# Optimization experiments

Measured on AMD Instinct MI355X. Metric: run time of the kernel, lower is better.

## Reference

```python
import jax, jax.numpy as jnp
import numpy as np

# Model dims (match init_kwargs / Mamba2 defaults)
D_MODEL = 1024
D_STATE = 128
D_CONV = 4
EXPAND = 2
HEADDIM = 64
NGROUPS = 1
D_INNER = EXPAND * D_MODEL            # 2048
NHEADS = D_INNER // HEADDIM           # 32
D_IN_PROJ = 2 * D_INNER + 2 * NGROUPS * D_STATE + NHEADS  # 4384 (d_mlp == 0)
CONV_DIM = D_INNER + 2 * NGROUPS * D_STATE                 # 2304
BATCH = 2
SEQLEN = 512
EPS = 1e-5


def _silu(x):
    return x * jax.nn.sigmoid(x)


def setup_inputs() -> dict:
    key = jax.random.key(0)
    ks = jax.random.split(key, 8)
    u = jax.random.normal(ks[0], (BATCH, SEQLEN, D_MODEL), jnp.float32)
    W_in = jax.random.normal(ks[1], (D_IN_PROJ, D_MODEL), jnp.float32) * (D_MODEL ** -0.5)
    conv_w = jax.random.normal(ks[2], (CONV_DIM, 1, D_CONV), jnp.float32) * (D_CONV ** -0.5)
    conv_b = jnp.zeros((CONV_DIM,), jnp.float32)
    # dt_bias init as in the torch module (inverse-softplus of dt in [dt_min, dt_max])
    dt = jnp.exp(jax.random.uniform(ks[3], (NHEADS,), jnp.float32)
                 * (np.log(0.1) - np.log(0.001)) + np.log(0.001))
    dt = jnp.clip(dt, 1e-4, None)
    dt_bias = dt + jnp.log(-jnp.expm1(-dt))
    A_log = jnp.log(jax.random.uniform(ks[4], (NHEADS,), jnp.float32, minval=1.0, maxval=16.0))
    D_param = jnp.ones((NHEADS,), jnp.float32)
    norm_w = jnp.ones((D_INNER,), jnp.float32)
    W_out = jax.random.normal(ks[5], (D_MODEL, D_INNER), jnp.float32) * (D_INNER ** -0.5)
    return dict(u=u, W_in=W_in, conv_w=conv_w, conv_b=conv_b, dt_bias=dt_bias,
                A_log=A_log, D_param=D_param, norm_w=norm_w, W_out=W_out)


def reference(u, W_in, conv_w, conv_b, dt_bias, A_log, D_param, norm_w, W_out):
    B, L, _ = u.shape
    # in_proj (no bias): [B,L,d_in_proj]
    zxbcdt = jnp.einsum('bld,ed->ble', u, W_in)
    z = zxbcdt[..., :D_INNER]
    xBC = zxbcdt[..., D_INNER:D_INNER + CONV_DIM]
    dt = zxbcdt[..., D_INNER + CONV_DIM:]          # [B,L,H]

    # causal depthwise conv1d (pad left d_conv-1 == conv padding + slice in torch)
    xc = jnp.transpose(xBC, (0, 2, 1))             # [B,C,L]
    xc = jax.lax.conv_general_dilated(
        xc, conv_w, window_strides=(1,), padding=[(D_CONV - 1, 0)],
        dimension_numbers=('NCH', 'OIH', 'NCH'), feature_group_count=CONV_DIM)
    xc = xc + conv_b[None, :, None]
    xBC = _silu(jnp.transpose(xc, (0, 2, 1)))      # [B,L,C]

    x = xBC[..., :D_INNER].reshape(B, L, NHEADS, HEADDIM)
    Bv = xBC[..., D_INNER:D_INNER + NGROUPS * D_STATE].reshape(B, L, NGROUPS, D_STATE)
    Cv = xBC[..., D_INNER + NGROUPS * D_STATE:].reshape(B, L, NGROUPS, D_STATE)

    A = -jnp.exp(A_log)                            # [H]
    dt = jax.nn.softplus(dt + dt_bias)             # [B,L,H]

    def step(state, inp):
        dt_t, x_t, B_t, C_t = inp                  # [B,H],[B,H,P],[B,G,N],[B,G,N]
        dA = jnp.exp(dt_t * A)                     # [B,H]
        dBx = jnp.einsum('bh,bgn,bhp->bhpn', dt_t, B_t, x_t)
        state = state * dA[:, :, None, None] + dBx
        y = jnp.einsum('bhpn,bgn->bhp', state, C_t) + D_param[:, None] * x_t
        return state, y

    state0 = jnp.zeros((B, NHEADS, HEADDIM, D_STATE), u.dtype)
    xs = (jnp.moveaxis(dt, 1, 0), jnp.moveaxis(x, 1, 0),
          jnp.moveaxis(Bv, 1, 0), jnp.moveaxis(Cv, 1, 0))
    _, ys = jax.lax.scan(step, state0, xs)         # ys: [L,B,H,P]
    y = jnp.moveaxis(ys, 0, 1).reshape(B, L, D_INNER)

    # RMSNormGated, norm_before_gate=False: gate first, then rmsnorm
    yg = y * _silu(z)
    yn = yg * jax.lax.rsqrt(jnp.mean(yg * yg, axis=-1, keepdims=True) + EPS) * norm_w

    return jnp.einsum('bld,ed->ble', yn, W_out)    # out_proj, no bias
```

## Files before the change

kernel.cpp:

```cpp
#include <hip/hip_runtime.h>
#include <hip/hip_bf16.h>

#define D_MODEL   1024
#define D_STATE   128
#define D_INNER   2048
#define NHEADS    32
#define HEADDIM   64
#define D_IN_PROJ 4384
#define NPROJ_PAD 4480
#define CONV_DIM  2304
#define BATCH     2
#define SEQLEN    512
#define M_TOKENS  (BATCH*SEQLEN)
#define EPS       1e-5f
#define LC        64
#define NCH       (SEQLEN/LC)

typedef __bf16 bf16x8 __attribute__((ext_vector_type(8)));
typedef float  f32x4  __attribute__((ext_vector_type(4)));

__device__ __forceinline__ ushort f2bf(float f) {
  union { float f; unsigned int i; } v; v.f = f;
  unsigned int x = v.i;
  return (ushort)((x + 0x7fffu + ((x >> 16) & 1u)) >> 16);
}
__device__ __forceinline__ float bf2f(ushort u) {
  union { unsigned int i; float f; } v; v.i = ((unsigned int)u) << 16; return v.f;
}

__device__ __forceinline__ void gload_lds16u(const ushort* g, ushort* l) {
  __builtin_amdgcn_global_load_lds(
      (const __attribute__((address_space(1))) void*)g,
      (__attribute__((address_space(3))) void*)l, 16, 0, 0);
}

__device__ __forceinline__ void cvt8(const float* __restrict__ s,
                                     ushort* __restrict__ d, int i) {
  const float4 a = *(const float4*)(s + i);
  const float4 b = *(const float4*)(s + i + 4);
  uint4 v;
  v.x = (unsigned)f2bf(a.x) | ((unsigned)f2bf(a.y) << 16);
  v.y = (unsigned)f2bf(a.z) | ((unsigned)f2bf(a.w) << 16);
  v.z = (unsigned)f2bf(b.x) | ((unsigned)f2bf(b.y) << 16);
  v.w = (unsigned)f2bf(b.z) | ((unsigned)f2bf(b.w) << 16);
  *(uint4*)(d + i) = v;
}
__global__ __launch_bounds__(256) void cvt3(const float* __restrict__ s0, ushort* __restrict__ d0, int n0,
                                            const float* __restrict__ s1, ushort* __restrict__ d1, int n1,
                                            const float* __restrict__ s2, ushort* __restrict__ d2, int n2,
                                            const float* __restrict__ nw) {
  const int i = (blockIdx.x * 256 + threadIdx.x) * 8;
  if (i < n0)           cvt8(s0, d0, i);
  else if (i < n0 + n1) cvt8(s1, d1, i - n0);
  else if (i < n0 + n1 + n2) {
    const int j = i - n0 - n1;
    const int k = j & (D_INNER - 1);
    const float4 a = *(const float4*)(s2 + j);
    const float4 b = *(const float4*)(s2 + j + 4);
    const float4 wa = *(const float4*)(nw + k);
    const float4 wb = *(const float4*)(nw + k + 4);
    uint4 v;
    v.x = (unsigned)f2bf(a.x * wa.x) | ((unsigned)f2bf(a.y * wa.y) << 16);
    v.y = (unsigned)f2bf(a.z * wa.z) | ((unsigned)f2bf(a.w * wa.w) << 16);
    v.z = (unsigned)f2bf(b.x * wb.x) | ((unsigned)f2bf(b.y * wb.y) << 16);
    v.w = (unsigned)f2bf(b.z * wb.z) | ((unsigned)f2bf(b.w * wb.w) << 16);
    *(uint4*)(d2 + j) = v;
  }
}

template <int BM, int BN, int MASK_N>
__global__ __launch_bounds__(256) void gemm_tile(const ushort* __restrict__ A,
                                                 const ushort* __restrict__ Bt,
                                                 float* __restrict__ C,
                                                 int Nreal, int K, int ldc) {
  constexpr int WM = BM / 2, WN = BN / 2, FM = WM / 16, FN = WN / 16;
  constexpr int LA = BM * 4 / 256, LB = BN * 4 / 256;
  __shared__ ushort As[BM * 32];
  __shared__ ushort Bs[BN * 32];
  const int tid = threadIdx.x, lane = tid & 63, wave = tid >> 6;
  const int r16 = lane & 15, q = lane >> 4;
  const int wm = wave & 1, wn = wave >> 1;
  const int m0 = blockIdx.y * BM, n0 = blockIdx.x * BN;

  f32x4 acc[FM][FN] = {};

  for (int k0 = 0; k0 < K; k0 += 32) {
    __syncthreads();
    #pragma unroll
    for (int it = 0; it < LA; ++it) {
      const int idx = it * 256 + tid;
      gload_lds16u(A + (size_t)(m0 + (idx >> 2)) * K + k0 + (idx & 3) * 8,
                   As + (it * 256 + wave * 64) * 8);
    }
    #pragma unroll
    for (int it = 0; it < LB; ++it) {
      const int idx = it * 256 + tid;
      gload_lds16u(Bt + (size_t)(n0 + (idx >> 2)) * K + k0 + (idx & 3) * 8,
                   Bs + (it * 256 + wave * 64) * 8);
    }
    __syncthreads();

    bf16x8 af[FM], bfr[FN];
    #pragma unroll
    for (int i = 0; i < FM; ++i)
      af[i] = *(const bf16x8*)(const void*)(As + (wm * WM + i * 16 + r16) * 32 + q * 8);
    #pragma unroll
    for (int j = 0; j < FN; ++j)
      bfr[j] = *(const bf16x8*)(const void*)(Bs + (wn * WN + j * 16 + r16) * 32 + q * 8);
    #pragma unroll
    for (int i = 0; i < FM; ++i)
      #pragma unroll
      for (int j = 0; j < FN; ++j)
        acc[i][j] = __builtin_amdgcn_mfma_f32_16x16x32_bf16(af[i], bfr[j], acc[i][j], 0, 0, 0);
  }

  #pragma unroll
  for (int i = 0; i < FM; ++i) {
    const int row = m0 + wm * WM + i * 16 + q * 4;
    #pragma unroll
    for (int j = 0; j < FN; ++j) {
      const int col = n0 + wn * WN + j * 16 + r16;
      if (!MASK_N || col < Nreal) {
        #pragma unroll
        for (int r = 0; r < 4; ++r)
          C[(size_t)(row + r) * ldc + col] = acc[i][j][r];
      }
    }
  }
}

__global__ __launch_bounds__(256) void gemm_sk(const ushort* __restrict__ A,
                                               const ushort* __restrict__ Bt,
                                               float* __restrict__ C,
                                               const float* __restrict__ sumsq,
                                               int Khalf, int ldab, int ldc) {
  __shared__ ushort As[64 * 32];
  __shared__ ushort Bs[64 * 32];
  const int tid = threadIdx.x, lane = tid & 63, wave = tid >> 6;
  const int r16 = lane & 15, q = lane >> 4;
  const int wm = wave & 1, wn = wave >> 1;
  const int m0 = blockIdx.y * 64, n0 = blockIdx.x * 64;
  const int kb = blockIdx.z * Khalf;

  f32x4 acc[2][2] = {};
  for (int k0 = 0; k0 < Khalf; k0 += 32) {
    __syncthreads();
    gload_lds16u(A + (size_t)(m0 + (tid >> 2)) * ldab + kb + k0 + (tid & 3) * 8,
                 As + (tid & ~63) * 8);
    gload_lds16u(Bt + (size_t)(n0 + (tid >> 2)) * ldab + kb + k0 + (tid & 3) * 8,
                 Bs + (tid & ~63) * 8);
    __syncthreads();

    bf16x8 af[2], bfr[2];
    #pragma unroll
    for (int i = 0; i < 2; ++i)
      af[i] = *(const bf16x8*)(const void*)(As + (wm * 32 + i * 16 + r16) * 32 + q * 8);
    #pragma unroll
    for (int j = 0; j < 2; ++j)
      bfr[j] = *(const bf16x8*)(const void*)(Bs + (wn * 32 + j * 16 + r16) * 32 + q * 8);
    #pragma unroll
    for (int i = 0; i < 2; ++i)
      #pragma unroll
      for (int j = 0; j < 2; ++j)
        acc[i][j] = __builtin_amdgcn_mfma_f32_16x16x32_bf16(af[i], bfr[j], acc[i][j], 0, 0, 0);
  }

  #pragma unroll
  for (int i = 0; i < 2; ++i) {
    const int row = m0 + wm * 32 + i * 16 + q * 4;
    float rms[4];
    #pragma unroll
    for (int r = 0; r < 4; ++r)
      rms[r] = rsqrtf(sumsq[row + r] * (1.f / D_INNER) + EPS);
    #pragma unroll
    for (int j = 0; j < 2; ++j) {
      const int col = n0 + wn * 32 + j * 16 + r16;
      #pragma unroll
      for (int r = 0; r < 4; ++r)
        unsafeAtomicAdd(&C[(size_t)(row + r) * ldc + col], acc[i][j][r] * rms[r]);
    }
  }
}

__global__ __launch_bounds__(256) void conv_dt(const float* __restrict__ zx,
                                               const float* __restrict__ cw,
                                               const float* __restrict__ cb,
                                               float* __restrict__ xbc,
                                               ushort* __restrict__ BCbf,
                                               const float* __restrict__ dt_bias,
                                               const float* __restrict__ A_log,
                                               float* __restrict__ dts,
                                               float* __restrict__ csum) {
  const int blk = blockIdx.x;
  if (blk < 1152) {
    const int g  = blk / 9;
    const int c  = (blk % 9) * 256 + threadIdx.x;
    const int b  = g >> 6;
    const int t0 = (g & 63) * 8;
    const float4 w4 = *(const float4*)(cw + c * 4);
    const float bias = cb[c];
    const float* col = zx + (size_t)(b * SEQLEN) * D_IN_PROJ + D_INNER + c;
    float win[11];
    #pragma unroll
    for (int k = 0; k < 11; ++k) {
      const int t = t0 - 3 + k;
      win[k] = (t >= 0) ? col[(size_t)t * D_IN_PROJ] : 0.f;
    }
    #pragma unroll
    for (int i = 0; i < 8; ++i) {
      float a = bias;
      a = fmaf(win[i],     w4.x, a);
      a = fmaf(win[i + 1], w4.y, a);
      a = fmaf(win[i + 2], w4.z, a);
      a = fmaf(win[i + 3], w4.w, a);
      const float s = a / (1.f + __expf(-a));
      const size_t bt = (size_t)(b * SEQLEN + t0 + i);
      xbc[bt * CONV_DIM + c] = s;
      if (c >= D_INNER) BCbf[bt * 256 + (c - D_INNER)] = f2bf(s);
    }
  } else {
    const int bh = blk - 1152;
    const int b = bh >> 5, h = bh & 31;
    const int wave = threadIdx.x >> 6, lane = threadIdx.x & 63;
    const float dtb = dt_bias[h];
    const float An  = -__expf(A_log[h]);
    for (int cc = wave; cc < NCH; cc += 4) {
      const int t = cc * LC + lane;
      const float raw = zx[(size_t)(b * SEQLEN + t) * D_IN_PROJ + (D_INNER + CONV_DIM) + h] + dtb;
      const float sp = (raw > 20.f) ? raw : log1pf(__expf(raw));
      float x = sp * An;
      #pragma unroll
      for (int off = 1; off < 64; off <<= 1) {
        const float v = __shfl_up(x, off);
        if (lane >= off) x += v;
      }
      dts[(size_t)bh * SEQLEN + t]  = sp;
      csum[(size_t)bh * SEQLEN + t] = x;
    }
  }
}

__global__ __launch_bounds__(256) void chunk_intra(const float* __restrict__ xbc,
                                                   const ushort* __restrict__ BCbf,
                                                   const float* __restrict__ dts,
                                                   const float* __restrict__ csum,
                                                   ushort* __restrict__ Yi,
                                                   ushort* __restrict__ dS) {
  const int blk = blockIdx.x;
  const int c = blk & 7, h = (blk >> 3) & 31, b = blk >> 8;
  const int bh = b * 32 + h;
  const int tid = threadIdx.x, lane = tid & 63, wave = tid >> 6;
  const int r16 = lane & 15, q = lane >> 4;

  __shared__ ushort Ml[64 * 72];
  __shared__ ushort Xt[64 * 72];
  __shared__ ushort Bw[128 * 72];
  __shared__ float dtl[LC], csl[LC];

  if (tid < LC) {
    dtl[tid] = dts[(size_t)bh * SEQLEN + c * LC + tid];
    csl[tid] = csum[(size_t)bh * SEQLEN + c * LC + tid];
  }
  __syncthreads();
  const float cs63 = csl[LC - 1];

  const ushort* Cp = BCbf + (size_t)(b * SEQLEN + c * LC + wave * 16 + r16) * 256 + 128 + q * 8;
  const ushort* Bp = BCbf + (size_t)(b * SEQLEN + c * LC + r16) * 256 + q * 8;
  f32x4 g[4] = {};
  #pragma unroll
  for (int kk = 0; kk < 4; ++kk) {
    const bf16x8 a = *(const bf16x8*)(const void*)(Cp + kk * 32);
    #pragma unroll
    for (int j = 0; j < 4; ++j) {
      const bf16x8 bb = *(const bf16x8*)(const void*)(Bp + (size_t)j * 16 * 256 + kk * 32);
      g[j] = __builtin_amdgcn_mfma_f32_16x16x32_bf16(a, bb, g[j], 0, 0, 0);
    }
  }
  float cst[4];
  #pragma unroll
  for (int r = 0; r < 4; ++r) cst[r] = csl[wave * 16 + q * 4 + r];
  #pragma unroll
  for (int j = 0; j < 4; ++j) {
    const int s = j * 16 + r16;
    const float ds_ = dtl[s], css = csl[s];
    #pragma unroll
    for (int r = 0; r < 4; ++r) {
      const int t = wave * 16 + q * 4 + r;
      const float v = (s <= t) ? g[j][r] * ds_ * __expf(cst[r] - css) : 0.f;
      Ml[t * 72 + s] = f2bf(v);
    }
  }

  const float* xb = xbc + (size_t)(b * SEQLEN + c * LC) * CONV_DIM + h * HEADDIM;
  #pragma unroll
  for (int i = 0; i < 16; ++i) {
    const int idx = i * 256 + tid;
    const int s = idx >> 6, p = idx & 63;
    Xt[p * 72 + s] = f2bf(xb[(size_t)s * CONV_DIM + p]);
  }
  const float* Bb = xbc + (size_t)(b * SEQLEN + c * LC) * CONV_DIM + D_INNER;
  #pragma unroll
  for (int i = 0; i < 32; ++i) {
    const int idx = i * 256 + tid;
    const int s = idx >> 7, n = idx & 127;
    const float w = dtl[s] * __expf(cs63 - csl[s]);
    Bw[n * 72 + s] = f2bf(Bb[(size_t)s * CONV_DIM + n] * w);
  }
  __syncthreads();

  f32x4 accY[4] = {};
  f32x4 accS[2][4] = {};
  #pragma unroll
  for (int kk = 0; kk < 2; ++kk) {
    const bf16x8 am = *(const bf16x8*)(const void*)(Ml + (wave * 16 + r16) * 72 + kk * 32 + q * 8);
    const bf16x8 a0 = *(const bf16x8*)(const void*)(Bw + (wave * 32 + r16) * 72 + kk * 32 + q * 8);
    const bf16x8 a1 = *(const bf16x8*)(const void*)(Bw + (wave * 32 + 16 + r16) * 72 + kk * 32 + q * 8);
    #pragma unroll
    for (int j = 0; j < 4; ++j) {
      const bf16x8 bx = *(const bf16x8*)(const void*)(Xt + (j * 16 + r16) * 72 + kk * 32 + q * 8);
      accY[j]    = __builtin_amdgcn_mfma_f32_16x16x32_bf16(am, bx, accY[j], 0, 0, 0);
      accS[0][j] = __builtin_amdgcn_mfma_f32_16x16x32_bf16(a0, bx, accS[0][j], 0, 0, 0);
      accS[1][j] = __builtin_amdgcn_mfma_f32_16x16x32_bf16(a1, bx, accS[1][j], 0, 0, 0);
    }
  }

  ushort* Yp = Yi + (size_t)blk * 4096;
  #pragma unroll
  for (int j = 0; j < 4; ++j)
    #pragma unroll
    for (int r = 0; r < 4; ++r)
      Yp[(wave * 16 + q * 4 + r) * 64 + j * 16 + r16] = f2bf(accY[j][r]);

  ushort* Sp = dS + (size_t)blk * 8192;
  #pragma unroll
  for (int u = 0; u < 2; ++u)
    #pragma unroll
    for (int j = 0; j < 4; ++j)
      #pragma unroll
      for (int r = 0; r < 4; ++r)
        Sp[(wave * 32 + u * 16 + q * 4 + r) * 64 + j * 16 + r16] = f2bf(accS[u][j][r]);
}

__global__ __launch_bounds__(256) void chunk_state(const ushort* __restrict__ dS,
                                                   const float* __restrict__ csum,
                                                   ushort* __restrict__ St) {
  const int bh = blockIdx.x;
  const int tid = threadIdx.x;
  const int p = tid & 63, n0 = (tid >> 6) * 32;
  float S[32] = {};
  for (int c = 0; c < NCH; ++c) {
    const size_t base = ((size_t)bh * 8 + c) * 8192;
    uint4 pk[4];
    unsigned* pw = (unsigned*)pk;
    #pragma unroll
    for (int j = 0; j < 16; ++j)
      pw[j] = (unsigned)f2bf(S[2 * j]) | ((unsigned)f2bf(S[2 * j + 1]) << 16);
    uint4* dst = (uint4*)(St + base + (size_t)p * 128 + n0);
    #pragma unroll
    for (int j = 0; j < 4; ++j) dst[j] = pk[j];
    const float e = __expf(csum[(size_t)bh * SEQLEN + c * LC + (LC - 1)]);
    #pragma unroll
    for (int j = 0; j < 32; ++j) {
      const float d = bf2f(dS[base + (size_t)(n0 + j) * 64 + p]);
      S[j] = S[j] * e + d;
    }
  }
}

__global__ __launch_bounds__(256) void chunk_inter(const ushort* __restrict__ BCbf,
                                                   const ushort* __restrict__ St,
                                                   const ushort* __restrict__ Yi,
                                                   const float* __restrict__ xbc,
                                                   const float* __restrict__ zx,
                                                   const float* __restrict__ csum,
                                                   const float* __restrict__ Dp,
                                                   ushort* __restrict__ yn,
                                                   float* __restrict__ sumsq) {
  const int blk = blockIdx.x;
  const int c = blk & 7, h = (blk >> 3) & 31, b = blk >> 8;
  const int bh = b * 32 + h;
  const int tid = threadIdx.x, lane = tid & 63, wave = tid >> 6;
  const int r16 = lane & 15, q = lane >> 4;

  const ushort* Cp = BCbf + (size_t)(b * SEQLEN + c * LC + wave * 16 + r16) * 256 + 128 + q * 8;
  const ushort* Sp = St + (size_t)blk * 8192 + (size_t)r16 * 128 + q * 8;
  f32x4 acc[4] = {};
  #pragma unroll
  for (int kk = 0; kk < 4; ++kk) {
    const bf16x8 a = *(const bf16x8*)(const void*)(Cp + kk * 32);
    #pragma unroll
    for (int j = 0; j < 4; ++j) {
      const bf16x8 bb = *(const bf16x8*)(const void*)(Sp + (size_t)j * 16 * 128 + kk * 32);
      acc[j] = __builtin_amdgcn_mfma_f32_16x16x32_bf16(a, bb, acc[j], 0, 0, 0);
    }
  }

  const float Dh = Dp[h];
  const ushort* Yp = Yi + (size_t)blk * 4096;
  float sc[4], ssq[4] = {0.f, 0.f, 0.f, 0.f};
  #pragma unroll
  for (int r = 0; r < 4; ++r)
    sc[r] = __expf(csum[(size_t)bh * SEQLEN + c * LC + wave * 16 + q * 4 + r]);
  #pragma unroll
  for (int j = 0; j < 4; ++j) {
    const int col = j * 16 + r16;
    #pragma unroll
    for (int r = 0; r < 4; ++r) {
      const int t = wave * 16 + q * 4 + r;
      const size_t row = (size_t)(b * SEQLEN + c * LC + t);
      const float xv = xbc[row * CONV_DIM + h * HEADDIM + col];
      const float yv = acc[j][r] * sc[r] + bf2f(Yp[t * 64 + col]) + Dh * xv;
      const float z  = zx[row * D_IN_PROJ + h * HEADDIM + col];
      const float yg = yv * (z / (1.f + __expf(-z)));
      yn[row * D_INNER + h * HEADDIM + col] = f2bf(yg);
      ssq[r] = fmaf(yg, yg, ssq[r]);
    }
  }
  #pragma unroll
  for (int o = 1; o < 16; o <<= 1) {
    #pragma unroll
    for (int r = 0; r < 4; ++r) ssq[r] += __shfl_xor(ssq[r], o);
  }
  if (r16 == 0) {
    #pragma unroll
    for (int r = 0; r < 4; ++r) {
      const int t = wave * 16 + q * 4 + r;
      unsafeAtomicAdd(&sumsq[b * SEQLEN + c * LC + t], ssq[r]);
    }
  }
}

extern "C" void kernel_launch(void* const* d_in, const int* in_sizes, int n_in,
                              void* d_out, int out_size, void* d_ws, size_t ws_size,
                              hipStream_t stream) {
  const float* u       = (const float*)d_in[0];
  const float* W_in    = (const float*)d_in[1];
  const float* conv_w  = (const float*)d_in[2];
  const float* conv_b  = (const float*)d_in[3];
  const float* dt_bias = (const float*)d_in[4];
  const float* A_log   = (const float*)d_in[5];
  const float* D_par   = (const float*)d_in[6];
  const float* norm_w  = (const float*)d_in[7];
  const float* W_out   = (const float*)d_in[8];
  float* out = (float*)d_out;

  char* ws = (char*)d_ws;
  float*  zx      = (float*)ws;
  float*  xbc     = (float*)(ws + 17956864);
  float*  sumsq   = (float*)(ws + 27394048);
  ushort* yn      = (ushort*)(ws + 35782656);
  ushort* u_bf    = (ushort*)(ws + 39976960);
  ushort* Win_bf  = (ushort*)(ws + 42074112);
  ushort* Yi      = (ushort*)(ws + 39976960);
  ushort* Wout_bf = (ushort*)(ws + 51052544);
  ushort* BC_bf   = (ushort*)(ws + 55246848);
  float*  dts     = (float*)(ws + 55771136);
  float*  csum    = (float*)(ws + 55902208);
  ushort* dS      = (ushort*)(ws + 56295424);
  ushort* St      = (ushort*)(ws + 64684032);

  hipMemsetAsync(out, 0, (size_t)M_TOKENS * D_MODEL * sizeof(float), stream);
  hipMemsetAsync(sumsq, 0, (size_t)M_TOKENS * sizeof(float), stream);

  const int n_u = M_TOKENS * D_MODEL, n_wi = D_IN_PROJ * D_MODEL, n_wo = D_MODEL * D_INNER;
  cvt3<<<(n_u + n_wi + n_wo) / (256 * 8), 256, 0, stream>>>(
      u, u_bf, n_u, W_in, Win_bf, n_wi, W_out, Wout_bf, n_wo, norm_w);

  gemm_tile<128, 64, 1><<<dim3(NPROJ_PAD / 64, M_TOKENS / 128), 256, 0, stream>>>(
      u_bf, Win_bf, zx, D_IN_PROJ, D_MODEL, D_IN_PROJ);
  conv_dt<<<1152 + 64, 256, 0, stream>>>(zx, conv_w, conv_b, xbc, BC_bf,
                                         dt_bias, A_log, dts, csum);

  chunk_intra<<<BATCH * NHEADS * NCH, 256, 0, stream>>>(xbc, BC_bf, dts, csum, Yi, dS);
  chunk_state<<<BATCH * NHEADS, 256, 0, stream>>>(dS, csum, St);
  chunk_inter<<<BATCH * NHEADS * NCH, 256, 0, stream>>>(BC_bf, St, Yi, xbc, zx,
                                                        csum, D_par, yn, sumsq);

  gemm_sk<<<dim3(D_MODEL / 64, M_TOKENS / 64, 2), 256, 0, stream>>>(
      yn, Wout_bf, out, sumsq, D_INNER / 2, D_INNER, D_MODEL);
}
```

Before: 188.9 us.

## Fold chunk-state recurrence into chunk_inter and double K-step in GEMMs

Measured after the change: 171.5 us. -9.2%, faster.

```diff
diff --git a/kernel.cpp b/kernel.cpp
--- a/kernel.cpp
+++ b/kernel.cpp
@@ -75,8 +75,8 @@
                                                  int Nreal, int K, int ldc) {
   constexpr int WM = BM / 2, WN = BN / 2, FM = WM / 16, FN = WN / 16;
   constexpr int LA = BM * 4 / 256, LB = BN * 4 / 256;
-  __shared__ ushort As[BM * 32];
-  __shared__ ushort Bs[BN * 32];
+  __shared__ ushort As[2 * BM * 32];
+  __shared__ ushort Bs[2 * BN * 32];
   const int tid = threadIdx.x, lane = tid & 63, wave = tid >> 6;
   const int r16 = lane & 15, q = lane >> 4;
   const int wm = wave & 1, wn = wave >> 1;
@@ -84,34 +84,40 @@
 
   f32x4 acc[FM][FN] = {};
 
-  for (int k0 = 0; k0 < K; k0 += 32) {
+  for (int k0 = 0; k0 < K; k0 += 64) {
     __syncthreads();
     #pragma unroll
-    for (int it = 0; it < LA; ++it) {
-      const int idx = it * 256 + tid;
-      gload_lds16u(A + (size_t)(m0 + (idx >> 2)) * K + k0 + (idx & 3) * 8,
-                   As + (it * 256 + wave * 64) * 8);
-    }
-    #pragma unroll
-    for (int it = 0; it < LB; ++it) {
-      const int idx = it * 256 + tid;
-      gload_lds16u(Bt + (size_t)(n0 + (idx >> 2)) * K + k0 + (idx & 3) * 8,
-                   Bs + (it * 256 + wave * 64) * 8);
+    for (int pp = 0; pp < 2; ++pp) {
+      #pragma unroll
+      for (int it = 0; it < LA; ++it) {
+        const int idx = it * 256 + tid;
+        gload_lds16u(A + (size_t)(m0 + (idx >> 2)) * K + k0 + pp * 32 + (idx & 3) * 8,
+                     As + pp * BM * 32 + (it * 256 + wave * 64) * 8);
+      }
+      #pragma unroll
+      for (int it = 0; it < LB; ++it) {
+        const int idx = it * 256 + tid;
+        gload_lds16u(Bt + (size_t)(n0 + (idx >> 2)) * K + k0 + pp * 32 + (idx & 3) * 8,
+                     Bs + pp * BN * 32 + (it * 256 + wave * 64) * 8);
+      }
     }
     __syncthreads();
 
-    bf16x8 af[FM], bfr[FN];
-    #pragma unroll
-    for (int i = 0; i < FM; ++i)
-      af[i] = *(const bf16x8*)(const void*)(As + (wm * WM + i * 16 + r16) * 32 + q * 8);
-    #pragma unroll
-    for (int j = 0; j < FN; ++j)
-      bfr[j] = *(const bf16x8*)(const void*)(Bs + (wn * WN + j * 16 + r16) * 32 + q * 8);
-    #pragma unroll
-    for (int i = 0; i < FM; ++i)
+    #pragma unroll
+    for (int pp = 0; pp < 2; ++pp) {
+      bf16x8 af[FM], bfr[FN];
+      #pragma unroll
+      for (int i = 0; i < FM; ++i)
+        af[i] = *(const bf16x8*)(const void*)(As + pp * BM * 32 + (wm * WM + i * 16 + r16) * 32 + q * 8);
       #pragma unroll
       for (int j = 0; j < FN; ++j)
-        acc[i][j] = __builtin_amdgcn_mfma_f32_16x16x32_bf16(af[i], bfr[j], acc[i][j], 0, 0, 0);
+        bfr[j] = *(const bf16x8*)(const void*)(Bs + pp * BN * 32 + (wn * WN + j * 16 + r16) * 32 + q * 8);
+      #pragma unroll
+      for (int i = 0; i < FM; ++i)
+        #pragma unroll
+        for (int j = 0; j < FN; ++j)
+          acc[i][j] = __builtin_amdgcn_mfma_f32_16x16x32_bf16(af[i], bfr[j], acc[i][j], 0, 0, 0);
+    }
   }
 
   #pragma unroll
@@ -134,8 +140,8 @@
                                                float* __restrict__ C,
                                                const float* __restrict__ sumsq,
                                                int Khalf, int ldab, int ldc) {
-  __shared__ ushort As[64 * 32];
-  __shared__ ushort Bs[64 * 32];
+  __shared__ ushort As[2 * 64 * 32];
+  __shared__ ushort Bs[2 * 64 * 32];
   const int tid = threadIdx.x, lane = tid & 63, wave = tid >> 6;
   const int r16 = lane & 15, q = lane >> 4;
   const int wm = wave & 1, wn = wave >> 1;
@@ -143,26 +149,32 @@
   const int kb = blockIdx.z * Khalf;
 
   f32x4 acc[2][2] = {};
-  for (int k0 = 0; k0 < Khalf; k0 += 32) {
+  for (int k0 = 0; k0 < Khalf; k0 += 64) {
     __syncthreads();
-    gload_lds16u(A + (size_t)(m0 + (tid >> 2)) * ldab + kb + k0 + (tid & 3) * 8,
-                 As + (tid & ~63) * 8);
-    gload_lds16u(Bt + (size_t)(n0 + (tid >> 2)) * ldab + kb + k0 + (tid & 3) * 8,
-                 Bs + (tid & ~63) * 8);
+    #pragma unroll
+    for (int pp = 0; pp < 2; ++pp) {
+      gload_lds16u(A + (size_t)(m0 + (tid >> 2)) * ldab + kb + k0 + pp * 32 + (tid & 3) * 8,
+                   As + pp * 64 * 32 + (tid & ~63) * 8);
+      gload_lds16u(Bt + (size_t)(n0 + (tid >> 2)) * ldab + kb + k0 + pp * 32 + (tid & 3) * 8,
+                   Bs + pp * 64 * 32 + (tid & ~63) * 8);
+    }
     __syncthreads();
 
-    bf16x8 af[2], bfr[2];
-    #pragma unroll
-    for (int i = 0; i < 2; ++i)
-      af[i] = *(const bf16x8*)(const void*)(As + (wm * 32 + i * 16 + r16) * 32 + q * 8);
-    #pragma unroll
-    for (int j = 0; j < 2; ++j)
-      bfr[j] = *(const bf16x8*)(const void*)(Bs + (wn * 32 + j * 16 + r16) * 32 + q * 8);
-    #pragma unroll
-    for (int i = 0; i < 2; ++i)
+    #pragma unroll
+    for (int pp = 0; pp < 2; ++pp) {
+      bf16x8 af[2], bfr[2];
+      #pragma unroll
+      for (int i = 0; i < 2; ++i)
+        af[i] = *(const bf16x8*)(const void*)(As + pp * 64 * 32 + (wm * 32 + i * 16 + r16) * 32 + q * 8);
       #pragma unroll
       for (int j = 0; j < 2; ++j)
-        acc[i][j] = __builtin_amdgcn_mfma_f32_16x16x32_bf16(af[i], bfr[j], acc[i][j], 0, 0, 0);
+        bfr[j] = *(const bf16x8*)(const void*)(Bs + pp * 64 * 32 + (wn * 32 + j * 16 + r16) * 32 + q * 8);
+      #pragma unroll
+      for (int i = 0; i < 2; ++i)
+        #pragma unroll
+        for (int j = 0; j < 2; ++j)
+          acc[i][j] = __builtin_amdgcn_mfma_f32_16x16x32_bf16(af[i], bfr[j], acc[i][j], 0, 0, 0);
+    }
   }
 
   #pragma unroll
@@ -341,34 +353,8 @@
         Sp[(wave * 32 + u * 16 + q * 4 + r) * 64 + j * 16 + r16] = f2bf(accS[u][j][r]);
 }
 
-__global__ __launch_bounds__(256) void chunk_state(const ushort* __restrict__ dS,
-                                                   const float* __restrict__ csum,
-                                                   ushort* __restrict__ St) {
-  const int bh = blockIdx.x;
-  const int tid = threadIdx.x;
-  const int p = tid & 63, n0 = (tid >> 6) * 32;
-  float S[32] = {};
-  for (int c = 0; c < NCH; ++c) {
-    const size_t base = ((size_t)bh * 8 + c) * 8192;
-    uint4 pk[4];
-    unsigned* pw = (unsigned*)pk;
-    #pragma unroll
-    for (int j = 0; j < 16; ++j)
-      pw[j] = (unsigned)f2bf(S[2 * j]) | ((unsigned)f2bf(S[2 * j + 1]) << 16);
-    uint4* dst = (uint4*)(St + base + (size_t)p * 128 + n0);
-    #pragma unroll
-    for (int j = 0; j < 4; ++j) dst[j] = pk[j];
-    const float e = __expf(csum[(size_t)bh * SEQLEN + c * LC + (LC - 1)]);
-    #pragma unroll
-    for (int j = 0; j < 32; ++j) {
-      const float d = bf2f(dS[base + (size_t)(n0 + j) * 64 + p]);
-      S[j] = S[j] * e + d;
-    }
-  }
-}
-
 __global__ __launch_bounds__(256) void chunk_inter(const ushort* __restrict__ BCbf,
-                                                   const ushort* __restrict__ St,
+                                                   const ushort* __restrict__ dS,
                                                    const ushort* __restrict__ Yi,
                                                    const float* __restrict__ xbc,
                                                    const float* __restrict__ zx,
@@ -382,15 +368,34 @@
   const int tid = threadIdx.x, lane = tid & 63, wave = tid >> 6;
   const int r16 = lane & 15, q = lane >> 4;
 
+  __shared__ ushort Stile[64 * 132];
+
+  const int p  = tid & 63;
+  const int n0 = (tid >> 6) * 32;
+  float S[32] = {};
+  float w = 1.f;
+  for (int cp = c - 1; cp >= 0; --cp) {
+    const ushort* dp = dS + ((size_t)bh * 8 + cp) * 8192 + (size_t)n0 * 64 + p;
+    #pragma unroll
+    for (int j = 0; j < 32; ++j)
+      S[j] = fmaf(w, bf2f(dp[(size_t)j * 64]), S[j]);
+    w *= __expf(csum[(size_t)bh * SEQLEN + cp * LC + (LC - 1)]);
+  }
+  #pragma unroll
+  for (int j = 0; j < 16; ++j) {
+    const unsigned v = (unsigned)f2bf(S[2 * j]) | ((unsigned)f2bf(S[2 * j + 1]) << 16);
+    *(unsigned*)&Stile[p * 132 + n0 + 2 * j] = v;
+  }
+  __syncthreads();
+
   const ushort* Cp = BCbf + (size_t)(b * SEQLEN + c * LC + wave * 16 + r16) * 256 + 128 + q * 8;
-  const ushort* Sp = St + (size_t)blk * 8192 + (size_t)r16 * 128 + q * 8;
   f32x4 acc[4] = {};
   #pragma unroll
   for (int kk = 0; kk < 4; ++kk) {
     const bf16x8 a = *(const bf16x8*)(const void*)(Cp + kk * 32);
     #pragma unroll
     for (int j = 0; j < 4; ++j) {
-      const bf16x8 bb = *(const bf16x8*)(const void*)(Sp + (size_t)j * 16 * 128 + kk * 32);
+      const bf16x8 bb = *(const bf16x8*)(const void*)(Stile + (j * 16 + r16) * 132 + kk * 32 + q * 8);
       acc[j] = __builtin_amdgcn_mfma_f32_16x16x32_bf16(a, bb, acc[j], 0, 0, 0);
     }
   }
@@ -457,7 +462,6 @@
   float*  dts     = (float*)(ws + 55771136);
   float*  csum    = (float*)(ws + 55902208);
   ushort* dS      = (ushort*)(ws + 56295424);
-  ushort* St      = (ushort*)(ws + 64684032);
 
   hipMemsetAsync(out, 0, (size_t)M_TOKENS * D_MODEL * sizeof(float), stream);
   hipMemsetAsync(sumsq, 0, (size_t)M_TOKENS * sizeof(float), stream);
@@ -472,8 +476,7 @@
                                          dt_bias, A_log, dts, csum);
 
   chunk_intra<<<BATCH * NHEADS * NCH, 256, 0, stream>>>(xbc, BC_bf, dts, csum, Yi, dS);
-  chunk_state<<<BATCH * NHEADS, 256, 0, stream>>>(dS, csum, St);
-  chunk_inter<<<BATCH * NHEADS * NCH, 256, 0, stream>>>(BC_bf, St, Yi, xbc, zx,
+  chunk_inter<<<BATCH * NHEADS * NCH, 256, 0, stream>>>(BC_bf, dS, Yi, xbc, zx,
                                                         csum, D_par, yn, sumsq);
 
   gemm_sk<<<dim3(D_MODEL / 64, M_TOKENS / 64, 2), 256, 0, stream>>>(
```
